# Kernel tuning notes

Hardware: AMD Instinct MI355X
Metric: run time of the kernel (lower is better)

Reference implementation:

```python
import jax, jax.numpy as jnp
import numpy as np
import math

NUM_HEADS = 8
DIM_EMBED = 640
DIM_CROSS = 768
DIM_HEAD = DIM_EMBED // NUM_HEADS


def setup_inputs() -> dict:
    key = jax.random.key(0)
    ks = jax.random.split(key, 10)
    B, SQ, SKV = 32, 1024, 77
    s_e = 1.0 / math.sqrt(DIM_EMBED)
    s_c = 1.0 / math.sqrt(DIM_CROSS)
    return {
        "x": jax.random.normal(ks[0], (B, SQ, DIM_EMBED), jnp.float32),
        "y": jax.random.normal(ks[1], (B, SKV, DIM_CROSS), jnp.float32),
        "Wq": jax.random.normal(ks[2], (DIM_EMBED, DIM_EMBED), jnp.float32) * s_e,
        "bq": jax.random.normal(ks[3], (DIM_EMBED,), jnp.float32) * 0.01,
        "Wk": jax.random.normal(ks[4], (DIM_CROSS, DIM_EMBED), jnp.float32) * s_c,
        "bk": jax.random.normal(ks[5], (DIM_EMBED,), jnp.float32) * 0.01,
        "Wv": jax.random.normal(ks[6], (DIM_CROSS, DIM_EMBED), jnp.float32) * s_c,
        "bv": jax.random.normal(ks[7], (DIM_EMBED,), jnp.float32) * 0.01,
        "Wo": jax.random.normal(ks[8], (DIM_EMBED, DIM_EMBED), jnp.float32) * s_e,
        "bo": jax.random.normal(ks[9], (DIM_EMBED,), jnp.float32) * 0.01,
    }


def reference(x, y, Wq, bq, Wk, bk, Wv, bv, Wo, bo):
    B, SQ, E = x.shape
    H, D = NUM_HEADS, DIM_HEAD
    q = x @ Wq + bq                      # [B, SQ, E]
    k = y @ Wk + bk                      # [B, SKV, E]
    v = y @ Wv + bv                      # [B, SKV, E]
    q = q.reshape(B, SQ, H, D)
    k = k.reshape(B, -1, H, D)
    v = v.reshape(B, -1, H, D)
    scores = jnp.einsum("bqhd,bkhd->bhqk", q, k) / math.sqrt(D)
    w = jax.nn.softmax(scores, axis=-1)
    out = jnp.einsum("bhqk,bkhd->bqhd", w, v).reshape(B, SQ, E)
    return out @ Wo + bo
```

## Files before the change

kernel.cpp:

```cpp
#include <hip/hip_runtime.h>
#include <hip/hip_bf16.h>

typedef __bf16 bf16x8 __attribute__((ext_vector_type(8)));
typedef float f32x4 __attribute__((ext_vector_type(4)));
typedef unsigned short us8 __attribute__((ext_vector_type(8)));
typedef unsigned int u32x4 __attribute__((ext_vector_type(4)));

#define E_ 640
#define CD_ 768
#define B_ 32
#define SQ_ 1024
#define SKV_ 77
#define H_ 8
#define DH_ 80

typedef __attribute__((address_space(3))) unsigned int as3_u32;
typedef __attribute__((address_space(1))) const unsigned int as1_u32;

__device__ __forceinline__ void gload16(const unsigned short* g, unsigned short* l) {
    __builtin_amdgcn_global_load_lds((as1_u32*)g, (as3_u32*)l, 16, 0, 0);
}

__device__ __forceinline__ float b2f(unsigned short u) {
    unsigned int x = ((unsigned int)u) << 16;
    return __builtin_bit_cast(float, x);
}
__device__ __forceinline__ unsigned short f2b(float f) {
    unsigned int x = __builtin_bit_cast(unsigned int, f);
    x += 0x7fffu + ((x >> 16) & 1u);
    return (unsigned short)(x >> 16);
}
__device__ __forceinline__ bf16x8 lv8(const unsigned short* p) {
    return __builtin_bit_cast(bf16x8, *reinterpret_cast<const us8*>(p));
}
__device__ __forceinline__ bf16x8 zero8() {
    us8 z = {0,0,0,0,0,0,0,0};
    return __builtin_bit_cast(bf16x8, z);
}
__device__ __forceinline__ bf16x8 cvtpk8(f32x4 lo, f32x4 hi) {
    unsigned int w0, w1, w2, w3;
    asm("v_cvt_pk_bf16_f32 %0, %1, %2" : "=v"(w0) : "v"(lo[0]), "v"(lo[1]));
    asm("v_cvt_pk_bf16_f32 %0, %1, %2" : "=v"(w1) : "v"(lo[2]), "v"(lo[3]));
    asm("v_cvt_pk_bf16_f32 %0, %1, %2" : "=v"(w2) : "v"(hi[0]), "v"(hi[1]));
    asm("v_cvt_pk_bf16_f32 %0, %1, %2" : "=v"(w3) : "v"(hi[2]), "v"(hi[3]));
    u32x4 w = {w0, w1, w2, w3};
    return __builtin_bit_cast(bf16x8, w);
}
__device__ __forceinline__ us8 cvt8(const float* s) {
    f32x4 f0 = *reinterpret_cast<const f32x4*>(s);
    f32x4 f1 = *reinterpret_cast<const f32x4*>(s + 4);
    return __builtin_bit_cast(us8, cvtpk8(f0, f1));
}

__device__ __forceinline__ void transpose_body(
    const float* __restrict__ in, unsigned short* __restrict__ out,
    int K, int N, int bx, int by, unsigned short (*t)[33])
{
    const int tx = threadIdx.x & 31, ty = threadIdx.x >> 5;
    const int n0 = bx * 32, k0 = by * 32;
#pragma unroll
    for (int i = 0; i < 4; ++i)
        t[ty + 8*i][tx] = f2b(in[(size_t)(k0 + ty + 8*i) * N + n0 + tx]);
    __syncthreads();
#pragma unroll
    for (int i = 0; i < 4; ++i)
        out[(size_t)(n0 + ty + 8*i) * K + k0 + tx] = t[tx][ty + 8*i];
}

__global__ __launch_bounds__(256) void fused_prep(
    const float* __restrict__ Wq, unsigned short* __restrict__ WqT,
    const float* __restrict__ Wo, unsigned short* __restrict__ WoT,
    const float* __restrict__ Wk, unsigned short* __restrict__ WkT,
    const float* __restrict__ Wv, unsigned short* __restrict__ WvT)
{
    __shared__ unsigned short t[32][33];
    const int id = blockIdx.x;
    if (id < 800) {
        int z = id / 400, rem = id % 400;
        transpose_body(z ? Wo : Wq, z ? WoT : WqT, 640, 640, rem % 20, rem / 20, t);
    } else {
        int id2 = id - 800, z = id2 / 480, rem = id2 % 480;
        transpose_body(z ? Wv : Wk, z ? WvT : WkT, 768, 640, rem % 20, rem / 20, t);
    }
}

template<int AMODE, bool CF32>
__device__ __forceinline__ void gemm_body(
    const void* __restrict__ Ap,
    const unsigned short* __restrict__ Wt,
    const float* __restrict__ bias,
    void* __restrict__ Cp,
    int M, int K, int ldc, int m0, int n0,
    unsigned short* smem)
{
    const int tid = threadIdx.x, lane = tid & 63, wave = tid >> 6;
    const int wr = (wave >> 1) << 6, wc = (wave & 1) << 6;
    const int l15 = lane & 15, l4 = lane >> 4;
    const int sgz = (tid >> 3) & 3;
    const int srd = (l15 >> 1) & 3;
    const int rdo = (l4 ^ srd) << 3;

    const unsigned short* gW0 = Wt + (size_t)(n0 + (tid >> 2)) * K + (((tid & 3) ^ sgz) << 3);
    const unsigned short* gW1 = Wt + (size_t)(n0 + (tid >> 2) + 64) * K + (((tid & 3) ^ sgz) << 3);

    const unsigned short* gA0; const unsigned short* gA1;
    const float* fA0; const float* fA1;
    int sw0, sw1;
    if constexpr (AMODE == 0) {
        gA0 = (const unsigned short*)Ap + (size_t)(m0 + (tid >> 2)) * K + (((tid & 3) ^ sgz) << 3);
        gA1 = (const unsigned short*)Ap + (size_t)(m0 + (tid >> 2) + 64) * K + (((tid & 3) ^ sgz) << 3);
    } else {
        int r0 = m0 + (tid >> 2); if (r0 >= M) r0 = M - 1;
        int r1 = r0 + 64; if (r1 >= M) r1 = M - 1;
        fA0 = (const float*)Ap + (size_t)r0 * K + (tid & 3) * 8;
        fA1 = (const float*)Ap + (size_t)r1 * K + (tid & 3) * 8;
        sw0 = ((tid & ~3) | ((tid & 3) ^ sgz)) * 8;
        sw1 = sw0 + 256 * 8;
    }

    f32x4 acc[4][4];
#pragma unroll
    for (int m = 0; m < 4; ++m)
#pragma unroll
        for (int n = 0; n < 4; ++n)
#pragma unroll
            for (int i = 0; i < 4; ++i) acc[m][n][i] = 0.f;

    auto STAGE = [&](int buf) {
        unsigned short* As = smem + buf * 8192;
        unsigned short* Ws = As + 4096;
        if constexpr (AMODE == 0) {
            gload16(gA0, As + tid * 8);
            gload16(gA1, As + (tid + 256) * 8);
            gA0 += 32; gA1 += 32;
        } else {
            *reinterpret_cast<us8*>(As + sw0) = cvt8(fA0);
            *reinterpret_cast<us8*>(As + sw1) = cvt8(fA1);
            fA0 += 32; fA1 += 32;
        }
        gload16(gW0, Ws + tid * 8);
        gload16(gW1, Ws + (tid + 256) * 8);
        gW0 += 32; gW1 += 32;
    };
    auto COMPUTE = [&](int buf) {
        const unsigned short* As = smem + buf * 8192;
        const unsigned short* Ws = As + 4096;
        bf16x8 a[4], b[4];
#pragma unroll
        for (int m = 0; m < 4; ++m)
            a[m] = lv8(&As[(wr + m * 16 + l15) * 32 + rdo]);
#pragma unroll
        for (int n = 0; n < 4; ++n)
            b[n] = lv8(&Ws[(wc + n * 16 + l15) * 32 + rdo]);
        __builtin_amdgcn_s_setprio(1);
#pragma unroll
        for (int m = 0; m < 4; ++m)
#pragma unroll
            for (int n = 0; n < 4; ++n)
                acc[m][n] = __builtin_amdgcn_mfma_f32_16x16x32_bf16(a[m], b[n], acc[m][n], 0, 0, 0);
        __builtin_amdgcn_s_setprio(0);
    };

    const int nk = K >> 5;
    STAGE(0);
    __syncthreads();
    for (int kt = 0; kt < nk - 2; kt += 2) {
        STAGE(1);
        COMPUTE(0);
        __syncthreads();
        STAGE(0);
        COMPUTE(1);
        __syncthreads();
    }
    STAGE(1);
    COMPUTE(0);
    __syncthreads();
    COMPUTE(1);

    float bs[4];
#pragma unroll
    for (int n = 0; n < 4; ++n) bs[n] = bias[n0 + wc + n * 16 + l15];

    if constexpr (CF32) {
        float* C = (float*)Cp;
        float* fs = (float*)smem;
#pragma unroll
        for (int p = 0; p < 2; ++p) {
            __syncthreads();
            if (wr == p * 64) {
#pragma unroll
                for (int m = 0; m < 4; ++m)
#pragma unroll
                    for (int n = 0; n < 4; ++n)
#pragma unroll
                        for (int i = 0; i < 4; ++i)
                            fs[(m * 16 + l4 * 4 + i) * 128 + wc + n * 16 + l15] =
                                acc[m][n][i] + bs[n];
            }
            __syncthreads();
#pragma unroll
            for (int r = 0; r < 8; ++r) {
                const int off = (r * 256 + tid) * 4;
                const int row = off >> 7, col = off & 127;
                const int grow = m0 + p * 64 + row;
                if (grow < M)
                    *reinterpret_cast<f32x4*>(&C[(size_t)grow * ldc + n0 + col]) =
                        *reinterpret_cast<const f32x4*>(&fs[off]);
            }
        }
    } else {
        unsigned short* C = (unsigned short*)Cp;
#pragma unroll
        for (int p = 0; p < 2; ++p) {
            __syncthreads();
            if (wr == p * 64) {
#pragma unroll
                for (int m = 0; m < 4; ++m)
#pragma unroll
                    for (int n = 0; n < 4; ++n)
#pragma unroll
                        for (int i = 0; i < 4; ++i)
                            smem[(m * 16 + l4 * 4 + i) * 128 + wc + n * 16 + l15] =
                                f2b(acc[m][n][i] + bs[n]);
            }
            __syncthreads();
#pragma unroll
            for (int r = 0; r < 4; ++r) {
                const int off = (r * 256 + tid) * 8;
                const int row = off >> 7, col = off & 127;
                const int grow = m0 + p * 64 + row;
                if (grow < M)
                    *reinterpret_cast<us8*>(&C[(size_t)grow * ldc + n0 + col]) =
                        *reinterpret_cast<us8*>(&smem[off]);
            }
        }
    }
}

__global__ __launch_bounds__(256) void fused_cvt_kv(
    const float* __restrict__ x, unsigned short* __restrict__ Xb,
    const float* __restrict__ y,
    const unsigned short* __restrict__ WkT, const float* __restrict__ bk2, unsigned short* __restrict__ Kb,
    const unsigned short* __restrict__ WvT, const float* __restrict__ bv2, unsigned short* __restrict__ Vb)
{
    __shared__ __align__(16) unsigned short smem[16384];
    const int id = blockIdx.x;
    if (id < 200) {
        int z = id / 100, rem = id % 100;
        int m0 = (rem / 5) * 128, n0 = (rem % 5) * 128;
        if (z == 0) gemm_body<1, false>(y, WkT, bk2, Kb, 2464, 768, 640, m0, n0, smem);
        else        gemm_body<1, false>(y, WvT, bv2, Vb, 2464, 768, 640, m0, n0, smem);
    } else {
        long i = (long)(id - 200) * 256 + threadIdx.x;
        const long stride = 2048L * 256;
        for (const long n8 = 2621440L; i < n8; i += stride)
            *reinterpret_cast<us8*>(Xb + i * 8) = cvt8(x + i * 8);
    }
}

__device__ __forceinline__ void vtrans_body(
    const unsigned short* __restrict__ Vb, unsigned short* __restrict__ Vt,
    int b, int h, unsigned short* Vl)
{
    const int tid = threadIdx.x;
    for (int idx = tid; idx < 770; idx += 256) {
        int kv = idx / 10, seg = idx % 10;
        *reinterpret_cast<us8*>(&Vl[kv * 88 + seg * 8]) =
            *reinterpret_cast<const us8*>(&Vb[(size_t)(b * 77 + kv) * 640 + h * 80 + seg * 8]);
    }
    __syncthreads();
    unsigned short* out = Vt + (size_t)(b * 8 + h) * 6400;
    for (int idx = tid; idx < 800; idx += 256) {
        int d = idx / 10, seg = idx % 10;
        us8 v;
#pragma unroll
        for (int j = 0; j < 8; ++j) {
            int kv = seg * 8 + j;
            v[j] = (kv < 77) ? Vl[kv * 88 + d] : (unsigned short)0;
        }
        *reinterpret_cast<us8*>(&out[d * 80 + seg * 8]) = v;
    }
}

__global__ __launch_bounds__(256) void fused_q_vt(
    const unsigned short* __restrict__ Xb, const unsigned short* __restrict__ WqT,
    const float* __restrict__ bq, unsigned short* __restrict__ Qb,
    const unsigned short* __restrict__ Vb, unsigned short* __restrict__ Vtb)
{
    __shared__ __align__(16) unsigned short smem[16384];
    const int id = blockIdx.x;
    if (id < 1280) {
        int wgid = (id & 7) * 160 + (id >> 3);
        int m0 = (wgid / 5) * 128, n0 = (wgid % 5) * 128;
        gemm_body<0, false>(Xb, WqT, bq, Qb, 32768, 640, 640, m0, n0, smem);
    } else {
        int r = id - 1280;
        vtrans_body(Vb, Vtb, r >> 3, r & 7, smem);
    }
}

__global__ __launch_bounds__(256) void gemm_o(
    const unsigned short* __restrict__ Ap, const unsigned short* __restrict__ Wt,
    const float* __restrict__ bias, float* __restrict__ Cp)
{
    __shared__ __align__(16) unsigned short smem[16384];
    const int orig = blockIdx.x;
    const int wgid = (orig & 7) * 160 + (orig >> 3);
    gemm_body<0, true>(Ap, Wt, bias, Cp, 32768, 640, 640,
                       (wgid / 5) * 128, (wgid % 5) * 128, smem);
}

__global__ __launch_bounds__(128) void attn_kernel(
    const unsigned short* __restrict__ Q,
    const unsigned short* __restrict__ Kp,
    const unsigned short* __restrict__ Vt,
    unsigned short* __restrict__ Oa)
{
    __shared__ __align__(16) unsigned short smem[11272];
    const int tid = threadIdx.x, lane = tid & 63, wave = tid >> 6;
    const int l15 = lane & 15, l4 = lane >> 4;
    const int qb = blockIdx.x * 128, h = blockIdx.y, b = blockIdx.z;
    const size_t qrow0 = (size_t)b * SQ_ + qb + wave * 64;
    const size_t kbase = (size_t)b * SKV_ * E_ + h * DH_;
    const size_t vbase = (size_t)(b * 8 + h) * 6400;

    bf16x8 aq[3][4];
#pragma unroll
    for (int ks = 0; ks < 3; ++ks) {
        const int d = ks * 32 + l4 * 8;
#pragma unroll
        for (int m = 0; m < 4; ++m)
            aq[ks][m] = (d < 80) ? lv8(&Q[(qrow0 + m * 16 + l15) * E_ + h * DH_ + d]) : zero8();
    }

    f32x4 accS[4][5];
#pragma unroll
    for (int m = 0; m < 4; ++m)
#pragma unroll
        for (int n = 0; n < 5; ++n)
#pragma unroll
            for (int i = 0; i < 4; ++i) accS[m][n][i] = 0.f;

#pragma unroll
    for (int ks = 0; ks < 3; ++ks) {
        const int d = ks * 32 + l4 * 8;
        bf16x8 bk[5];
#pragma unroll
        for (int n = 0; n < 5; ++n) {
            const int kv = n * 16 + l15;
            bk[n] = (kv < SKV_ && d < 80) ? lv8(&Kp[kbase + (size_t)kv * E_ + d]) : zero8();
        }
        __builtin_amdgcn_s_setprio(1);
#pragma unroll
        for (int n = 0; n < 5; ++n)
#pragma unroll
            for (int m = 0; m < 4; ++m)
                accS[m][n] = __builtin_amdgcn_mfma_f32_16x16x32_bf16(aq[ks][m], bk[n], accS[m][n], 0, 0, 0);
        __builtin_amdgcn_s_setprio(0);
    }

    unsigned short* Pw = smem + wave * 5632;

    const float scale = 0.11180339887498949f;
    float rs[4][4];
#pragma unroll
    for (int m = 0; m < 4; ++m) {
#pragma unroll
        for (int i = 0; i < 4; ++i) {
            float mx = -1e30f;
#pragma unroll
            for (int n = 0; n < 5; ++n) {
                float s = accS[m][n][i] * scale;
                if (n == 4 && l15 >= 13) s = -1e30f;
                accS[m][n][i] = s;
                mx = fmaxf(mx, s);
            }
            mx = fmaxf(mx, __shfl_xor(mx, 1));
            mx = fmaxf(mx, __shfl_xor(mx, 2));
            mx = fmaxf(mx, __shfl_xor(mx, 4));
            mx = fmaxf(mx, __shfl_xor(mx, 8));
            float sum = 0.f;
            const int prow = m * 16 + l4 * 4 + i;
#pragma unroll
            for (int n = 0; n < 5; ++n) {
                float p = __expf(accS[m][n][i] - mx);
                sum += p;
                Pw[prow * 88 + n * 16 + l15] = f2b(p);
            }
            sum += __shfl_xor(sum, 1);
            sum += __shfl_xor(sum, 2);
            sum += __shfl_xor(sum, 4);
            sum += __shfl_xor(sum, 8);
            rs[m][i] = sum;
        }
    }

    f32x4 accO[4][5];
#pragma unroll
    for (int m = 0; m < 4; ++m)
#pragma unroll
        for (int n = 0; n < 5; ++n)
#pragma unroll
            for (int i = 0; i < 4; ++i) accO[m][n][i] = 0.f;

#pragma unroll
    for (int ks = 0; ks < 3; ++ks) {
        const int kv = ks * 32 + l4 * 8;
        bf16x8 ap[4], bv[5];
#pragma unroll
        for (int m = 0; m < 4; ++m)
            ap[m] = (ks < 2 || l4 < 2) ? lv8(&Pw[(m * 16 + l15) * 88 + ks * 32 + l4 * 8])
                                       : zero8();
#pragma unroll
        for (int n = 0; n < 5; ++n) {
            const int d = n * 16 + l15;
            bv[n] = (kv < 80) ? lv8(&Vt[vbase + (size_t)d * 80 + kv]) : zero8();
        }
        __builtin_amdgcn_s_setprio(1);
#pragma unroll
        for (int n = 0; n < 5; ++n)
#pragma unroll
            for (int m = 0; m < 4; ++m)
                accO[m][n] = __builtin_amdgcn_mfma_f32_16x16x32_bf16(ap[m], bv[n], accO[m][n], 0, 0, 0);
        __builtin_amdgcn_s_setprio(0);
    }

    __syncthreads();
#pragma unroll
    for (int m = 0; m < 4; ++m) {
#pragma unroll
        for (int i = 0; i < 4; ++i) {
            const float inv = 1.f / rs[m][i];
            const int rl = wave * 64 + m * 16 + l4 * 4 + i;
#pragma unroll
            for (int n = 0; n < 5; ++n)
                smem[rl * 80 + n * 16 + l15] = f2b(accO[m][n][i] * inv);
        }
    }
    __syncthreads();
    const size_t obase = (size_t)b * SQ_ + qb;
    for (int idx = tid; idx < 1280; idx += 128) {
        int row = idx / 10, seg = idx % 10;
        *reinterpret_cast<us8*>(&Oa[(obase + row) * E_ + h * DH_ + seg * 8]) =
            *reinterpret_cast<us8*>(&smem[row * 80 + seg * 8]);
    }
}

extern "C" void kernel_launch(void* const* d_in, const int* in_sizes, int n_in,
                              void* d_out, int out_size, void* d_ws, size_t ws_size,
                              hipStream_t stream) {
    const float* x  = (const float*)d_in[0];
    const float* y  = (const float*)d_in[1];
    const float* Wq = (const float*)d_in[2];
    const float* bq = (const float*)d_in[3];
    const float* Wk = (const float*)d_in[4];
    const float* bk = (const float*)d_in[5];
    const float* Wv = (const float*)d_in[6];
    const float* bv = (const float*)d_in[7];
    const float* Wo = (const float*)d_in[8];
    const float* bo = (const float*)d_in[9];
    float* out = (float*)d_out;

    char* ws = (char*)d_ws;
    unsigned short* WqT = (unsigned short*)(ws + 0);
    unsigned short* WkT = (unsigned short*)(ws + 819200);
    unsigned short* WvT = (unsigned short*)(ws + 1802240);
    unsigned short* WoT = (unsigned short*)(ws + 2785280);
    unsigned short* Qb  = (unsigned short*)(ws + 3604480);
    unsigned short* Kb  = (unsigned short*)(ws + 45547520);
    unsigned short* Vb  = (unsigned short*)(ws + 48701440);
    unsigned short* Xb  = (unsigned short*)(ws + 51855360);
    unsigned short* Vtb = (unsigned short*)(ws + 93798400);

    fused_prep<<<1760, 256, 0, stream>>>(Wq, WqT, Wo, WoT, Wk, WkT, Wv, WvT);
    fused_cvt_kv<<<2248, 256, 0, stream>>>(x, Xb, y, WkT, bk, Kb, WvT, bv, Vb);
    fused_q_vt<<<1536, 256, 0, stream>>>(Xb, WqT, bq, Qb, Vb, Vtb);
    attn_kernel<<<dim3(8, 8, 32), 128, 0, stream>>>(Qb, Kb, Vtb, Qb);
    gemm_o<<<1280, 256, 0, stream>>>(Qb, WoT, bo, out);
}
```

Before: 177.2 us.

## Use triple-buffered LDS pipeline with one barrier per k-step for bf16 GEMMs

Splits the shared GEMM body into a bf16-input version used by the Q and output projections and a separate fp32-input version for the K/V projection. The bf16 version moves to three LDS buffers, issues loads two stages ahead, and uses explicit vmcnt waits with a single barrier per k-step instead of two. The goal is to hide global-to-LDS load latency behind MFMA work and cut barrier stalls. The cost is 48KB of LDS per block instead of 32KB, which may reduce occupancy.

New measurement: 159.0 us. -10.3%, faster.

```diff
diff --git a/kernel.cpp b/kernel.cpp
--- a/kernel.cpp
+++ b/kernel.cpp
@@ -84,9 +84,9 @@
     }
 }
 
-template<int AMODE, bool CF32>
-__device__ __forceinline__ void gemm_body(
-    const void* __restrict__ Ap,
+template<bool CF32>
+__device__ __forceinline__ void gemm_pipe(
+    const unsigned short* __restrict__ A,
     const unsigned short* __restrict__ Wt,
     const float* __restrict__ bias,
     void* __restrict__ Cp,
@@ -102,21 +102,8 @@
 
     const unsigned short* gW0 = Wt + (size_t)(n0 + (tid >> 2)) * K + (((tid & 3) ^ sgz) << 3);
     const unsigned short* gW1 = Wt + (size_t)(n0 + (tid >> 2) + 64) * K + (((tid & 3) ^ sgz) << 3);
-
-    const unsigned short* gA0; const unsigned short* gA1;
-    const float* fA0; const float* fA1;
-    int sw0, sw1;
-    if constexpr (AMODE == 0) {
-        gA0 = (const unsigned short*)Ap + (size_t)(m0 + (tid >> 2)) * K + (((tid & 3) ^ sgz) << 3);
-        gA1 = (const unsigned short*)Ap + (size_t)(m0 + (tid >> 2) + 64) * K + (((tid & 3) ^ sgz) << 3);
-    } else {
-        int r0 = m0 + (tid >> 2); if (r0 >= M) r0 = M - 1;
-        int r1 = r0 + 64; if (r1 >= M) r1 = M - 1;
-        fA0 = (const float*)Ap + (size_t)r0 * K + (tid & 3) * 8;
-        fA1 = (const float*)Ap + (size_t)r1 * K + (tid & 3) * 8;
-        sw0 = ((tid & ~3) | ((tid & 3) ^ sgz)) * 8;
-        sw1 = sw0 + 256 * 8;
-    }
+    const unsigned short* gA0 = A + (size_t)(m0 + (tid >> 2)) * K + (((tid & 3) ^ sgz) << 3);
+    const unsigned short* gA1 = A + (size_t)(m0 + (tid >> 2) + 64) * K + (((tid & 3) ^ sgz) << 3);
 
     f32x4 acc[4][4];
 #pragma unroll
@@ -129,15 +116,142 @@
     auto STAGE = [&](int buf) {
         unsigned short* As = smem + buf * 8192;
         unsigned short* Ws = As + 4096;
-        if constexpr (AMODE == 0) {
-            gload16(gA0, As + tid * 8);
-            gload16(gA1, As + (tid + 256) * 8);
-            gA0 += 32; gA1 += 32;
-        } else {
-            *reinterpret_cast<us8*>(As + sw0) = cvt8(fA0);
-            *reinterpret_cast<us8*>(As + sw1) = cvt8(fA1);
-            fA0 += 32; fA1 += 32;
-        }
+        gload16(gA0, As + tid * 8);
+        gload16(gA1, As + (tid + 256) * 8);
+        gload16(gW0, Ws + tid * 8);
+        gload16(gW1, Ws + (tid + 256) * 8);
+        gA0 += 32; gA1 += 32; gW0 += 32; gW1 += 32;
+    };
+    auto COMPUTE = [&](int buf) {
+        const unsigned short* As = smem + buf * 8192;
+        const unsigned short* Ws = As + 4096;
+        bf16x8 a[4], b[4];
+#pragma unroll
+        for (int m = 0; m < 4; ++m)
+            a[m] = lv8(&As[(wr + m * 16 + l15) * 32 + rdo]);
+#pragma unroll
+        for (int n = 0; n < 4; ++n)
+            b[n] = lv8(&Ws[(wc + n * 16 + l15) * 32 + rdo]);
+        __builtin_amdgcn_s_setprio(1);
+#pragma unroll
+        for (int m = 0; m < 4; ++m)
+#pragma unroll
+            for (int n = 0; n < 4; ++n)
+                acc[m][n] = __builtin_amdgcn_mfma_f32_16x16x32_bf16(a[m], b[n], acc[m][n], 0, 0, 0);
+        __builtin_amdgcn_s_setprio(0);
+    };
+
+    const int nk = K >> 5;
+    STAGE(0);
+    STAGE(1);
+    for (int t = 0; t < nk; ++t) {
+        if (t == nk - 1) { asm volatile("s_waitcnt vmcnt(0)" ::: "memory"); }
+        else             { asm volatile("s_waitcnt vmcnt(4)" ::: "memory"); }
+        __builtin_amdgcn_sched_barrier(0);
+        __builtin_amdgcn_s_barrier();
+        COMPUTE(t % 3);
+        if (t + 2 < nk) STAGE((t + 2) % 3);
+    }
+
+    float bs[4];
+#pragma unroll
+    for (int n = 0; n < 4; ++n) bs[n] = bias[n0 + wc + n * 16 + l15];
+
+    if constexpr (CF32) {
+        float* C = (float*)Cp;
+        float* fs = (float*)smem;
+#pragma unroll
+        for (int p = 0; p < 2; ++p) {
+            __syncthreads();
+            if (wr == p * 64) {
+#pragma unroll
+                for (int m = 0; m < 4; ++m)
+#pragma unroll
+                    for (int n = 0; n < 4; ++n)
+#pragma unroll
+                        for (int i = 0; i < 4; ++i)
+                            fs[(m * 16 + l4 * 4 + i) * 128 + wc + n * 16 + l15] =
+                                acc[m][n][i] + bs[n];
+            }
+            __syncthreads();
+#pragma unroll
+            for (int r = 0; r < 8; ++r) {
+                const int off = (r * 256 + tid) * 4;
+                const int row = off >> 7, col = off & 127;
+                const int grow = m0 + p * 64 + row;
+                if (grow < M)
+                    *reinterpret_cast<f32x4*>(&C[(size_t)grow * ldc + n0 + col]) =
+                        *reinterpret_cast<const f32x4*>(&fs[off]);
+            }
+        }
+    } else {
+        unsigned short* C = (unsigned short*)Cp;
+#pragma unroll
+        for (int p = 0; p < 2; ++p) {
+            __syncthreads();
+            if (wr == p * 64) {
+#pragma unroll
+                for (int m = 0; m < 4; ++m)
+#pragma unroll
+                    for (int n = 0; n < 4; ++n)
+#pragma unroll
+                        for (int i = 0; i < 4; ++i)
+                            smem[(m * 16 + l4 * 4 + i) * 128 + wc + n * 16 + l15] =
+                                f2b(acc[m][n][i] + bs[n]);
+            }
+            __syncthreads();
+#pragma unroll
+            for (int r = 0; r < 4; ++r) {
+                const int off = (r * 256 + tid) * 8;
+                const int row = off >> 7, col = off & 127;
+                const int grow = m0 + p * 64 + row;
+                if (grow < M)
+                    *reinterpret_cast<us8*>(&C[(size_t)grow * ldc + n0 + col]) =
+                        *reinterpret_cast<us8*>(&smem[off]);
+            }
+        }
+    }
+}
+
+__device__ __forceinline__ void gemm_kv_body(
+    const float* __restrict__ Ap,
+    const unsigned short* __restrict__ Wt,
+    const float* __restrict__ bias,
+    unsigned short* __restrict__ Cp,
+    int M, int K, int ldc, int m0, int n0,
+    unsigned short* smem)
+{
+    const int tid = threadIdx.x, lane = tid & 63, wave = tid >> 6;
+    const int wr = (wave >> 1) << 6, wc = (wave & 1) << 6;
+    const int l15 = lane & 15, l4 = lane >> 4;
+    const int sgz = (tid >> 3) & 3;
+    const int srd = (l15 >> 1) & 3;
+    const int rdo = (l4 ^ srd) << 3;
+
+    const unsigned short* gW0 = Wt + (size_t)(n0 + (tid >> 2)) * K + (((tid & 3) ^ sgz) << 3);
+    const unsigned short* gW1 = Wt + (size_t)(n0 + (tid >> 2) + 64) * K + (((tid & 3) ^ sgz) << 3);
+
+    int r0 = m0 + (tid >> 2); if (r0 >= M) r0 = M - 1;
+    int r1 = r0 + 64; if (r1 >= M) r1 = M - 1;
+    const float* fA0 = Ap + (size_t)r0 * K + (tid & 3) * 8;
+    const float* fA1 = Ap + (size_t)r1 * K + (tid & 3) * 8;
+    const int sw0 = ((tid & ~3) | ((tid & 3) ^ sgz)) * 8;
+    const int sw1 = sw0 + 256 * 8;
+
+    f32x4 acc[4][4];
+#pragma unroll
+    for (int m = 0; m < 4; ++m)
+#pragma unroll
+        for (int n = 0; n < 4; ++n)
+#pragma unroll
+            for (int i = 0; i < 4; ++i) acc[m][n][i] = 0.f;
+
+    auto STAGE = [&](int buf) {
+        unsigned short* As = smem + buf * 8192;
+        unsigned short* Ws = As + 4096;
+        *reinterpret_cast<us8*>(As + sw0) = cvt8(fA0);
+        *reinterpret_cast<us8*>(As + sw1) = cvt8(fA1);
+        fA0 += 32; fA1 += 32;
         gload16(gW0, Ws + tid * 8);
         gload16(gW1, Ws + (tid + 256) * 8);
         gW0 += 32; gW1 += 32;
@@ -181,58 +295,28 @@
 #pragma unroll
     for (int n = 0; n < 4; ++n) bs[n] = bias[n0 + wc + n * 16 + l15];
 
-    if constexpr (CF32) {
-        float* C = (float*)Cp;
-        float* fs = (float*)smem;
-#pragma unroll
-        for (int p = 0; p < 2; ++p) {
-            __syncthreads();
-            if (wr == p * 64) {
-#pragma unroll
-                for (int m = 0; m < 4; ++m)
-#pragma unroll
-                    for (int n = 0; n < 4; ++n)
-#pragma unroll
-                        for (int i = 0; i < 4; ++i)
-                            fs[(m * 16 + l4 * 4 + i) * 128 + wc + n * 16 + l15] =
-                                acc[m][n][i] + bs[n];
-            }
-            __syncthreads();
-#pragma unroll
-            for (int r = 0; r < 8; ++r) {
-                const int off = (r * 256 + tid) * 4;
-                const int row = off >> 7, col = off & 127;
-                const int grow = m0 + p * 64 + row;
-                if (grow < M)
-                    *reinterpret_cast<f32x4*>(&C[(size_t)grow * ldc + n0 + col]) =
-                        *reinterpret_cast<const f32x4*>(&fs[off]);
-            }
-        }
-    } else {
-        unsigned short* C = (unsigned short*)Cp;
-#pragma unroll
-        for (int p = 0; p < 2; ++p) {
-            __syncthreads();
-            if (wr == p * 64) {
-#pragma unroll
-                for (int m = 0; m < 4; ++m)
-#pragma unroll
-                    for (int n = 0; n < 4; ++n)
-#pragma unroll
-                        for (int i = 0; i < 4; ++i)
-                            smem[(m * 16 + l4 * 4 + i) * 128 + wc + n * 16 + l15] =
-                                f2b(acc[m][n][i] + bs[n]);
-            }
-            __syncthreads();
-#pragma unroll
-            for (int r = 0; r < 4; ++r) {
-                const int off = (r * 256 + tid) * 8;
-                const int row = off >> 7, col = off & 127;
-                const int grow = m0 + p * 64 + row;
-                if (grow < M)
-                    *reinterpret_cast<us8*>(&C[(size_t)grow * ldc + n0 + col]) =
-                        *reinterpret_cast<us8*>(&smem[off]);
-            }
+#pragma unroll
+    for (int p = 0; p < 2; ++p) {
+        __syncthreads();
+        if (wr == p * 64) {
+#pragma unroll
+            for (int m = 0; m < 4; ++m)
+#pragma unroll
+                for (int n = 0; n < 4; ++n)
+#pragma unroll
+                    for (int i = 0; i < 4; ++i)
+                        smem[(m * 16 + l4 * 4 + i) * 128 + wc + n * 16 + l15] =
+                            f2b(acc[m][n][i] + bs[n]);
+        }
+        __syncthreads();
+#pragma unroll
+        for (int r = 0; r < 4; ++r) {
+            const int off = (r * 256 + tid) * 8;
+            const int row = off >> 7, col = off & 127;
+            const int grow = m0 + p * 64 + row;
+            if (grow < M)
+                *reinterpret_cast<us8*>(&Cp[(size_t)grow * ldc + n0 + col]) =
+                    *reinterpret_cast<us8*>(&smem[off]);
         }
     }
 }
@@ -248,8 +332,8 @@
     if (id < 200) {
         int z = id / 100, rem = id % 100;
         int m0 = (rem / 5) * 128, n0 = (rem % 5) * 128;
-        if (z == 0) gemm_body<1, false>(y, WkT, bk2, Kb, 2464, 768, 640, m0, n0, smem);
-        else        gemm_body<1, false>(y, WvT, bv2, Vb, 2464, 768, 640, m0, n0, smem);
+        if (z == 0) gemm_kv_body(y, WkT, bk2, Kb, 2464, 768, 640, m0, n0, smem);
+        else        gemm_kv_body(y, WvT, bv2, Vb, 2464, 768, 640, m0, n0, smem);
     } else {
         long i = (long)(id - 200) * 256 + threadIdx.x;
         const long stride = 2048L * 256;
@@ -287,12 +371,12 @@
     const float* __restrict__ bq, unsigned short* __restrict__ Qb,
     const unsigned short* __restrict__ Vb, unsigned short* __restrict__ Vtb)
 {
-    __shared__ __align__(16) unsigned short smem[16384];
+    __shared__ __align__(16) unsigned short smem[24576];
     const int id = blockIdx.x;
     if (id < 1280) {
         int wgid = (id & 7) * 160 + (id >> 3);
         int m0 = (wgid / 5) * 128, n0 = (wgid % 5) * 128;
-        gemm_body<0, false>(Xb, WqT, bq, Qb, 32768, 640, 640, m0, n0, smem);
+        gemm_pipe<false>(Xb, WqT, bq, Qb, 32768, 640, 640, m0, n0, smem);
     } else {
         int r = id - 1280;
         vtrans_body(Vb, Vtb, r >> 3, r & 7, smem);
@@ -303,11 +387,11 @@
     const unsigned short* __restrict__ Ap, const unsigned short* __restrict__ Wt,
     const float* __restrict__ bias, float* __restrict__ Cp)
 {
-    __shared__ __align__(16) unsigned short smem[16384];
+    __shared__ __align__(16) unsigned short smem[24576];
     const int orig = blockIdx.x;
     const int wgid = (orig & 7) * 160 + (orig >> 3);
-    gemm_body<0, true>(Ap, Wt, bias, Cp, 32768, 640, 640,
-                       (wgid / 5) * 128, (wgid % 5) * 128, smem);
+    gemm_pipe<true>(Ap, Wt, bias, Cp, 32768, 640, 640,
+                    (wgid / 5) * 128, (wgid % 5) * 128, smem);
 }
 
 __global__ __launch_bounds__(128) void attn_kernel(
```
